# Kernel optimization log

Measured on AMD Instinct MI355X. Metric: run time of the kernel, lower is better.

Reference implementation:

```python
import jax, jax.numpy as jnp
import numpy as np

B, S, D, H = 2, 2048, 2048, 16
HD = D // H  # 128
THETA = 10000.0


def _rope_cos_sin(seq_len, head_dim):
    # matches LlamaRotaryEmbedding: inv_freq = 1/theta^(2i/d), emb = cat(freqs, freqs)
    inv_freq = 1.0 / (THETA ** (jnp.arange(0, head_dim, 2, dtype=jnp.float32) / head_dim))
    t = jnp.arange(seq_len, dtype=jnp.float32)
    freqs = jnp.einsum('s,d->sd', t, inv_freq)          # [S, HD/2]
    emb = jnp.concatenate([freqs, freqs], axis=-1)       # [S, HD]
    return jnp.cos(emb), jnp.sin(emb)


def _rotate_half(x):
    x1, x2 = jnp.split(x, 2, axis=-1)
    return jnp.concatenate([-x2, x1], axis=-1)


def setup_inputs() -> dict:
    key = jax.random.key(0)
    ks = jax.random.split(key, 5)
    scale = D ** -0.5
    x = jax.random.normal(ks[0], (B, S, D), jnp.float32)
    wq = jax.random.normal(ks[1], (D, D), jnp.float32) * scale
    wk = jax.random.normal(ks[2], (D, D), jnp.float32) * scale
    wv = jax.random.normal(ks[3], (D, D), jnp.float32) * scale
    wo = jax.random.normal(ks[4], (D, D), jnp.float32) * scale
    # additive causal mask (0 on/below diagonal, large negative above)
    causal = jnp.tril(jnp.ones((S, S), dtype=bool))
    mask = jnp.where(causal, 0.0, -1e9).astype(jnp.float32)[None, None]  # [1,1,S,S]
    return {"x": x, "wq": wq, "wk": wk, "wv": wv, "wo": wo, "mask": mask}


def reference(x, wq, wk, wv, wo, mask):
    b, s, d = x.shape
    # projections + head split: [b, H, s, HD]
    q = (x @ wq).reshape(b, s, H, HD).transpose(0, 2, 1, 3)
    k = (x @ wk).reshape(b, s, H, HD).transpose(0, 2, 1, 3)
    v = (x @ wv).reshape(b, s, H, HD).transpose(0, 2, 1, 3)
    # inline RoPE on q and k (positions 0..s-1 along the seq axis)
    cos, sin = _rope_cos_sin(s, HD)
    cos = cos[None, None]  # [1,1,s,HD]
    sin = sin[None, None]
    q = q * cos + _rotate_half(q) * sin
    k = k * cos + _rotate_half(k) * sin
    # eager attention: QK^T * scale + mask -> softmax -> @ V
    attn = jnp.einsum('bhqd,bhkd->bhqk', q, k) * (HD ** -0.5)
    attn = jax.nn.softmax(attn + mask, axis=-1)
    out = jnp.einsum('bhqk,bhkd->bhqd', attn, v)
    out = out.transpose(0, 2, 1, 3).reshape(b, s, d)
    return out @ wo
```

## Files before the change

### kernel.cpp

```cpp
#include <hip/hip_runtime.h>

#define S_LEN 2048
#define D_DIM 2048
#define NH 16
#define HD 128
#define NB 2
#define NROW (NB * S_LEN)
#define QKV_STR 6144

typedef unsigned short bf16;
typedef __attribute__((ext_vector_type(8))) short bf16x8;
typedef __attribute__((ext_vector_type(4))) float f32x4;
typedef __attribute__((ext_vector_type(16))) float f32x16;
typedef __attribute__((address_space(3))) unsigned int as3u;
typedef __attribute__((address_space(1))) unsigned int as1u;

__device__ __forceinline__ void gload16(const void* g, void* l) {
  __builtin_amdgcn_global_load_lds((const as1u*)g, (as3u*)l, 16, 0, 0);
}

__device__ __forceinline__ unsigned short f2bf(float f) {
  unsigned u = __builtin_bit_cast(unsigned, f);
  u += 0x7FFFu + ((u >> 16) & 1u);
  return (unsigned short)(u >> 16);
}
__device__ __forceinline__ float bf2f(unsigned short b) {
  return __builtin_bit_cast(float, (unsigned)b << 16);
}
__device__ __forceinline__ unsigned cvtpk(float lo, float hi) {
  unsigned r;
  asm("v_cvt_pk_bf16_f32 %0, %1, %2" : "=v"(r) : "v"(lo), "v"(hi));
  return r;
}
__device__ __forceinline__ float exp2a(float x) {
  float r;
  asm("v_exp_f32 %0, %1" : "=v"(r) : "v"(x));
  return r;
}


__global__ void rope_table_k(float2* __restrict__ tab) {
  int i = blockIdx.x * 256 + threadIdx.x;
  int s = i >> 6, d = i & 63;
  float invf = powf(10000.0f, -(float)d * (1.0f / 64.0f));
  float ang = (float)s * invf;
  tab[i] = make_float2(cosf(ang), sinf(ang));
}

__global__ void convert_x_k(const float* __restrict__ src, bf16* __restrict__ dst) {
  int i = (blockIdx.x * 256 + threadIdx.x) * 4;
  float4 v = *(const float4*)(src + i);
  ushort4 w;
  w.x = f2bf(v.x); w.y = f2bf(v.y); w.z = f2bf(v.z); w.w = f2bf(v.w);
  *(ushort4*)(dst + i) = w;
}

__global__ void transpose_w_k(const float* __restrict__ W, bf16* __restrict__ Wt) {
  __shared__ float t[64][65];
  int c0 = blockIdx.x * 64, r0 = blockIdx.y * 64;
  int tx = threadIdx.x & 63, ty = threadIdx.x >> 6;
#pragma unroll
  for (int i = 0; i < 16; ++i)
    t[ty + i * 4][tx] = W[(size_t)(r0 + ty + i * 4) * D_DIM + c0 + tx];
  __syncthreads();
#pragma unroll
  for (int i = 0; i < 16; ++i)
    Wt[(size_t)(c0 + ty + i * 4) * D_DIM + r0 + tx] = f2bf(t[tx][ty + i * 4]);
}

__global__ void transpose_v_k(const bf16* __restrict__ Vsrc, bf16* __restrict__ Vt) {
  __shared__ bf16 t[64][65];
  int bh = blockIdx.z;
  int b = bh >> 4, h = bh & 15;
  int s0 = blockIdx.x * 64, d0 = blockIdx.y * 64;
  int tx = threadIdx.x & 63, ty = threadIdx.x >> 6;
  const bf16* src = Vsrc + (size_t)(b * S_LEN + s0) * QKV_STR + h * HD + d0;
#pragma unroll
  for (int i = 0; i < 16; ++i)
    t[ty + i * 4][tx] = src[(size_t)(ty + i * 4) * QKV_STR + tx];
  __syncthreads();
  bf16* dst = Vt + ((size_t)bh * HD + d0) * S_LEN + s0;
#pragma unroll
  for (int i = 0; i < 16; ++i)
    dst[(size_t)(ty + i * 4) * S_LEN + tx] = t[tx][ty + i * 4];
}

__global__ void rope_apply_k(bf16* __restrict__ qkv, const float2* __restrict__ tab) {
  int i = blockIdx.x * 256 + threadIdx.x;
  int d = i & 63;
  int t = i >> 6;
  int h = t & 15;
  int row = t >> 4;
  int s = row & (S_LEN - 1);
  const float qscale = 0.12751743f;
  float2 cs = tab[s * 64 + d];
  size_t base = (size_t)row * QKV_STR + h * HD + d;
  float x1 = bf2f(qkv[base]), x2 = bf2f(qkv[base + 64]);
  qkv[base]      = f2bf((x1 * cs.x - x2 * cs.y) * qscale);
  qkv[base + 64] = f2bf((x2 * cs.x + x1 * cs.y) * qscale);
  size_t kb2 = base + 2048;
  float y1 = bf2f(qkv[kb2]), y2 = bf2f(qkv[kb2 + 64]);
  qkv[kb2]      = f2bf(y1 * cs.x - y2 * cs.y);
  qkv[kb2 + 64] = f2bf(y2 * cs.x + y1 * cs.y);
}


__device__ __forceinline__ void storec(bf16* p, float v) { *p = f2bf(v); }
__device__ __forceinline__ void storec(float* p, float v) { *p = v; }

template <typename OutT>
__global__ __launch_bounds__(256) void gemm_bt_k(
    const bf16* __restrict__ A, const bf16* __restrict__ Bt,
    OutT* __restrict__ C, int M, int N, int K) {
  __shared__ bf16 As[128 * 64];
  __shared__ bf16 Bs[128 * 64];
  const int tid = threadIdx.x;
  const int lane = tid & 63;
  const int wid = tid >> 6;
  const int bm = blockIdx.y * 128;
  const int bn = blockIdx.x * 128;
  const int wr = (wid >> 1) * 64;
  const int wc = (wid & 1) * 64;
  const int lr = lane & 15;
  const int kg = lane >> 4;

  f32x4 acc[4][4] = {};

  const int srow = lane >> 3;
  const int scol = ((lane & 7) ^ srow) * 8;
  const bf16* Ap = A + (size_t)(bm + wid * 32 + srow) * K + scol;
  const bf16* Bp = Bt + (size_t)(bn + wid * 32 + srow) * K + scol;
  bf16* Asd = &As[wid * 32 * 64];
  bf16* Bsd = &Bs[wid * 32 * 64];

  const int rx = (lr & 7) << 4;

  for (int k0 = 0; k0 < K; k0 += 64) {
    __syncthreads();
#pragma unroll
    for (int p = 0; p < 4; ++p) {
      gload16(Ap + (size_t)(p * 8) * K + k0, Asd + p * 8 * 64);
      gload16(Bp + (size_t)(p * 8) * K + k0, Bsd + p * 8 * 64);
    }
    __syncthreads();
    bf16x8 a[4][2], b[4][2];
#pragma unroll
    for (int m = 0; m < 4; ++m) {
      const char* rowp = (const char*)&As[(wr + m * 16 + lr) * 64];
#pragma unroll
      for (int kk = 0; kk < 2; ++kk)
        a[m][kk] = *(const bf16x8*)(rowp + ((kk * 64 + kg * 16) ^ rx));
    }
#pragma unroll
    for (int n = 0; n < 4; ++n) {
      const char* rowp = (const char*)&Bs[(wc + n * 16 + lr) * 64];
#pragma unroll
      for (int kk = 0; kk < 2; ++kk)
        b[n][kk] = *(const bf16x8*)(rowp + ((kk * 64 + kg * 16) ^ rx));
    }
#pragma unroll
    for (int kk = 0; kk < 2; ++kk)
#pragma unroll
      for (int m = 0; m < 4; ++m)
#pragma unroll
        for (int n = 0; n < 4; ++n)
          acc[m][n] = __builtin_amdgcn_mfma_f32_16x16x32_bf16(a[m][kk], b[n][kk], acc[m][n], 0, 0, 0);
  }

#pragma unroll
  for (int m = 0; m < 4; ++m) {
    int row0 = bm + wr + m * 16 + kg * 4;
#pragma unroll
    for (int n = 0; n < 4; ++n) {
      int col = bn + wc + n * 16 + lr;
#pragma unroll
      for (int r = 0; r < 4; ++r)
        storec(&C[(size_t)(row0 + r) * N + col], acc[m][n][r]);
    }
  }
}

#define FBODY(T, CUR0, CUR1, NXT0, NXT1)                                         \
  {                                                                              \
    const int kv0_ = (T) * 64;                                                   \
    stageV(kv0_ + 64, ((T) + 1) & 1);                                            \
    stageK(kv0_ + 192, kb_st);                                                   \
    kb_st = (kb_st == 2) ? 0 : kb_st + 1;                                        \
    if (kv0_ + 64 <= qw0 + 31) {                                                 \
      NXT0 = 0.0f; NXT1 = 0.0f;                                                  \
      const bf16* krow0_ = &sh[kb_rd * 8192] + (size_t)l31 * 128;                \
      const bf16* krow1_ = krow0_ + 32 * 128;                                    \
      _Pragma("unroll")                                                          \
      for (int ks = 0; ks < 8; ++ks) {                                           \
        int cb_ = ((ks * 32) ^ kxor) >> 1;                                       \
        bf16x8 kf0_ = *(const bf16x8*)(krow0_ + cb_);                            \
        bf16x8 kf1_ = *(const bf16x8*)(krow1_ + cb_);                            \
        NXT0 = __builtin_amdgcn_mfma_f32_32x32x16_bf16(kf0_, qf[ks], NXT0, 0, 0, 0); \
        NXT1 = __builtin_amdgcn_mfma_f32_32x32x16_bf16(kf1_, qf[ks], NXT1, 0, 0, 0); \
      }                                                                          \
    }                                                                            \
    kb_rd = (kb_rd == 2) ? 0 : kb_rd + 1;                                        \
    if (kv0_ <= qw0 + 31) {                                                      \
      if (kv0_ + 63 > qw0) {                                                     \
        _Pragma("unroll")                                                        \
        for (int r = 0; r < 16; ++r) {                                           \
          int kvg_ = kv0_ + (r & 3) + 8 * (r >> 2) + 4 * h;                      \
          if (kvg_ > q) CUR0[r] = -3.0e38f;                                      \
          if (kvg_ + 32 > q) CUR1[r] = -3.0e38f;                                 \
        }                                                                        \
      }                                                                          \
      float tm_[8];                                                              \
      _Pragma("unroll")                                                          \
      for (int r = 0; r < 8; ++r)                                                \
        tm_[r] = fmaxf(fmaxf(CUR0[r], CUR0[r + 8]), fmaxf(CUR1[r], CUR1[r + 8])); \
      _Pragma("unroll")                                                          \
      for (int r = 0; r < 4; ++r) tm_[r] = fmaxf(tm_[r], tm_[r + 4]);            \
      float mt_ = fmaxf(fmaxf(tm_[0], tm_[1]), fmaxf(tm_[2], tm_[3]));           \
      mt_ = fmaxf(mt_, __shfl_xor(mt_, 32));                                     \
      if (__any(mt_ > m_run + 8.0f)) {                                           \
        float mnew_ = fmaxf(m_run, mt_);                                         \
        float alpha_ = exp2a(m_run - mnew_);                                     \
        l_run *= alpha_;                                                         \
        _Pragma("unroll")                                                        \
        for (int n = 0; n < 4; ++n)                                              \
          _Pragma("unroll")                                                      \
          for (int r = 0; r < 16; ++r) ot[n][r] *= alpha_;                       \
        m_run = mnew_;                                                           \
      }                                                                          \
      float rs_[16];                                                             \
      _Pragma("unroll")                                                          \
      for (int r = 0; r < 16; ++r) {                                             \
        CUR0[r] = exp2a(CUR0[r] - m_run);                                        \
        CUR1[r] = exp2a(CUR1[r] - m_run);                                        \
        rs_[r] = CUR0[r] + CUR1[r];                                              \
      }                                                                          \
      _Pragma("unroll")                                                          \
      for (int r = 0; r < 8; ++r) rs_[r] += rs_[r + 8];                          \
      _Pragma("unroll")                                                          \
      for (int r = 0; r < 4; ++r) rs_[r] += rs_[r + 4];                          \
      float rsum_ = (rs_[0] + rs_[1]) + (rs_[2] + rs_[3]);                       \
      rsum_ += __shfl_xor(rsum_, 32);                                            \
      l_run += rsum_;                                                            \
      unsigned wd0_[8], wd1_[8];                                                 \
      _Pragma("unroll")                                                          \
      for (int j = 0; j < 8; ++j) {                                              \
        wd0_[j] = cvtpk(CUR0[2 * j], CUR0[2 * j + 1]);                           \
        wd1_[j] = cvtpk(CUR1[2 * j], CUR1[2 * j + 1]);                           \
      }                                                                          \
      const bf16* Vbuf_ = &sh[24576 + ((T) & 1) * 8192];                         \
      _Pragma("unroll")                                                          \
      for (int t4 = 0; t4 < 4; ++t4) {                                           \
        const unsigned* wdp_ = (t4 >> 1) ? wd1_ : wd0_;                          \
        int a0_ = 4 * (t4 & 1) + 2 * h;                                          \
        int sidx_ = 4 * (t4 & 1) + 2 * (1 - h);                                  \
        unsigned s0_ = (unsigned)__shfl_xor((int)wdp_[sidx_], 32);               \
        unsigned s1_ = (unsigned)__shfl_xor((int)wdp_[sidx_ + 1], 32);           \
        unsigned pb4_[4];                                                        \
        pb4_[0] = h ? s0_ : wdp_[a0_];                                           \
        pb4_[1] = h ? s1_ : wdp_[a0_ + 1];                                       \
        pb4_[2] = h ? wdp_[a0_] : s0_;                                           \
        pb4_[3] = h ? wdp_[a0_ + 1] : s1_;                                       \
        bf16x8 pb_ = __builtin_bit_cast(bf16x8, *(uint4*)pb4_);                  \
        int cb_ = ((t4 * 32) ^ vxor) >> 1;                                       \
        _Pragma("unroll")                                                        \
        for (int n = 0; n < 4; ++n) {                                            \
          bf16x8 va_ = *(const bf16x8*)(Vbuf_ + (size_t)(32 * n + l31) * 64 + cb_); \
          ot[n] = __builtin_amdgcn_mfma_f32_32x32x16_bf16(va_, pb_, ot[n], 0, 0, 0); \
        }                                                                        \
      }                                                                          \
    }                                                                            \
    asm volatile("s_waitcnt vmcnt(4)" ::: "memory");                             \
    __builtin_amdgcn_sched_barrier(0);                                           \
    __builtin_amdgcn_s_barrier();                                                \
  }

__global__ __launch_bounds__(256, 2) void flash_attn_k(
    const bf16* __restrict__ Q, const bf16* __restrict__ Kb,
    const bf16* __restrict__ Vt, bf16* __restrict__ O) {
  __shared__ bf16 sh[40960];
  const int tid = threadIdx.x;
  const int lane = tid & 63;
  const int w = tid >> 6;
  const int h = lane >> 5;
  const int l31 = lane & 31;
  const int bh = blockIdx.y;
  const int b = bh >> 4;
  const int hh = bh & 15;
  const int xr = (bh & 16) ? blockIdx.x : (gridDim.x - 1 - blockIdx.x);
  const int qb = xr * 128;
  const int qw0 = qb + 32 * w;
  const int q = qw0 + l31;

  const bf16* qp = Q + (size_t)(b * S_LEN + q) * QKV_STR + hh * HD + h * 8;
  bf16x8 qf[8];
#pragma unroll
  for (int ks = 0; ks < 8; ++ks) qf[ks] = *(const bf16x8*)(qp + ks * 16);

  f32x16 ot[4] = {};
  float m_run = -3.0e38f, l_run = 0.f;

  const bf16* Kg = Kb + (size_t)(b * S_LEN) * QKV_STR + hh * HD;
  const bf16* Vg = Vt + (size_t)bh * HD * S_LEN;

  const int kst_row = 16 * w + (lane >> 4);
  const int vst_row = 32 * w + (lane >> 3);
  const int vst_col = (((lane & 7) ^ (lane >> 3)) << 3);
  const int kxor = (16 * h) ^ ((l31 & 15) << 4);
  const int vxor = (16 * h) ^ ((l31 & 7) << 4);

  auto stageK = [&](int kv0, int buf) {
#pragma unroll
    for (int jj = 0; jj < 4; ++jj) {
      int kr = (kv0 + kst_row + jj * 4) & (S_LEN - 1);
      gload16(Kg + (size_t)kr * QKV_STR + (((lane & 15) ^ (jj * 4 + (lane >> 4))) << 3),
              &sh[buf * 8192 + (16 * w + jj * 4) * 128]);
    }
  };
  auto stageV = [&](int kv0, int buf) {
    int c = (kv0 & (S_LEN - 1)) + vst_col;
#pragma unroll
    for (int jj = 0; jj < 4; ++jj) {
      int vr = vst_row + jj * 8;
      gload16(Vg + (size_t)vr * S_LEN + c, &sh[24576 + buf * 8192 + (32 * w + jj * 8) * 64]);
    }
  };

  stageK(0, 0);
  stageV(0, 0);
  stageK(64, 1);
  stageK(128, 2);
  asm volatile("s_waitcnt vmcnt(12)" ::: "memory");
  __builtin_amdgcn_sched_barrier(0);
  __builtin_amdgcn_s_barrier();

  f32x16 stA0 = 0.0f, stA1 = 0.0f, stB0, stB1;
  {
    const bf16* krow0 = &sh[0] + (size_t)l31 * 128;
    const bf16* krow1 = krow0 + 32 * 128;
#pragma unroll
    for (int ks = 0; ks < 8; ++ks) {
      int cb = ((ks * 32) ^ kxor) >> 1;
      bf16x8 kf0 = *(const bf16x8*)(krow0 + cb);
      bf16x8 kf1 = *(const bf16x8*)(krow1 + cb);
      stA0 = __builtin_amdgcn_mfma_f32_32x32x16_bf16(kf0, qf[ks], stA0, 0, 0, 0);
      stA1 = __builtin_amdgcn_mfma_f32_32x32x16_bf16(kf1, qf[ks], stA1, 0, 0, 0);
    }
  }
  asm volatile("s_waitcnt vmcnt(4)" ::: "memory");
  __builtin_amdgcn_sched_barrier(0);
  __builtin_amdgcn_s_barrier();

  int kb_st = 0;
  int kb_rd = 1;
  const int nt = qb / 64 + 2;
  int t = 0;
  for (; t + 1 < nt; t += 2) {
    FBODY(t, stA0, stA1, stB0, stB1);
    FBODY(t + 1, stB0, stB1, stA0, stA1);
  }
  if (t < nt) FBODY(t, stA0, stA1, stB0, stB1);

  asm volatile("s_waitcnt vmcnt(0)" ::: "memory");
  __builtin_amdgcn_s_barrier();

  float inv = 1.0f / l_run;
  bf16* ow = &sh[w * 4096];
#pragma unroll
  for (int n = 0; n < 4; ++n)
#pragma unroll
    for (int rq = 0; rq < 4; ++rq) {
      int dbase = 32 * n + 8 * rq + 4 * h;
      unsigned u0 = cvtpk(ot[n][4 * rq + 0] * inv, ot[n][4 * rq + 1] * inv);
      unsigned u1 = cvtpk(ot[n][4 * rq + 2] * inv, ot[n][4 * rq + 3] * inv);
      uint2 uu = make_uint2(u0, u1);
      *(uint2*)(ow + l31 * 128 + (dbase ^ ((l31 & 15) << 3))) = uu;
    }
  __syncthreads();
#pragma unroll
  for (int p = 0; p < 8; ++p) {
    int qr = p * 4 + (lane >> 4);
    int ce = ((((lane & 15) << 4) ^ ((qr & 15) << 4)) >> 1);
    bf16x8 vrow = *(const bf16x8*)(ow + qr * 128 + ce);
    *(bf16x8*)(O + (size_t)(b * S_LEN + qw0 + qr) * D_DIM + hh * HD + (lane & 15) * 8) = vrow;
  }
}


extern "C" void kernel_launch(void* const* d_in, const int* in_sizes, int n_in,
                              void* d_out, int out_size, void* d_ws, size_t ws_size,
                              hipStream_t stream) {
  (void)in_sizes; (void)n_in; (void)out_size; (void)ws_size;
  const float* x  = (const float*)d_in[0];
  const float* wq = (const float*)d_in[1];
  const float* wk = (const float*)d_in[2];
  const float* wv = (const float*)d_in[3];
  const float* wo = (const float*)d_in[4];
  float* out = (float*)d_out;

  char* ws = (char*)d_ws;
  const size_t MB = 1u << 20;
  bf16* xb    = (bf16*)(ws + 0 * MB);
  bf16* Ob    = xb;
  bf16* wTall = (bf16*)(ws + 16 * MB);
  bf16* wTo   = (bf16*)(ws + 40 * MB);
  bf16* QKV   = (bf16*)(ws + 48 * MB);
  bf16* Vtb   = (bf16*)(ws + 96 * MB);
  float2* tab = (float2*)(ws + 112 * MB);

  rope_table_k<<<512, 256, 0, stream>>>(tab);
  convert_x_k<<<8192, 256, 0, stream>>>(x, xb);
  dim3 tg(32, 32);
  transpose_w_k<<<tg, 256, 0, stream>>>(wq, wTall);
  transpose_w_k<<<tg, 256, 0, stream>>>(wk, wTall + (size_t)2048 * D_DIM);
  transpose_w_k<<<tg, 256, 0, stream>>>(wv, wTall + (size_t)4096 * D_DIM);
  transpose_w_k<<<tg, 256, 0, stream>>>(wo, wTo);

  gemm_bt_k<bf16><<<dim3(QKV_STR / 128, NROW / 128), 256, 0, stream>>>(
      xb, wTall, QKV, NROW, QKV_STR, D_DIM);

  rope_apply_k<<<16384, 256, 0, stream>>>(QKV, tab);
  transpose_v_k<<<dim3(32, 2, 32), 256, 0, stream>>>(QKV + 4096, Vtb);

  flash_attn_k<<<dim3(S_LEN / 128, NB * NH), 256, 0, stream>>>(
      QKV, QKV + 2048, Vtb, Ob);

  gemm_bt_k<float><<<dim3(D_DIM / 128, NROW / 128), 256, 0, stream>>>(
      Ob, wTo, out, NROW, D_DIM, D_DIM);
}
```

Measured before the change: 312.1 us.

## Fuse RoPE and V transpose into QKV GEMM epilogue; batch weight transposes

Adds a dedicated QKV GEMM whose epilogue applies RoPE (plus the softmax scale on Q) and writes V straight out in transposed layout. This removes the separate rope_apply and transpose_v kernels and their extra round trips through global memory. Each warp's columns are remapped so that d and d+64 land in the same thread, which lets the rotation run in registers. The four weight-transpose launches are merged into one 3D grid launch. The V epilogue writes 4-element packed stores strided by S_LEN, and the RoPE epilogue reads the table per element, so stores may be less coalesced.

```diff
diff --git a/kernel.cpp b/kernel.cpp
--- a/kernel.cpp
+++ b/kernel.cpp
@@ -55,8 +55,13 @@
   *(ushort4*)(dst + i) = w;
 }
 
-__global__ void transpose_w_k(const float* __restrict__ W, bf16* __restrict__ Wt) {
+__global__ void transpose_w_k(const float* __restrict__ w0, const float* __restrict__ w1,
+                              const float* __restrict__ w2, const float* __restrict__ w3,
+                              bf16* __restrict__ wTall, bf16* __restrict__ wTo) {
   __shared__ float t[64][65];
+  int z = blockIdx.z;
+  const float* W = (z == 0) ? w0 : (z == 1) ? w1 : (z == 2) ? w2 : w3;
+  bf16* Wt = (z == 3) ? wTo : wTall + (size_t)z * 2048 * D_DIM;
   int c0 = blockIdx.x * 64, r0 = blockIdx.y * 64;
   int tx = threadIdx.x & 63, ty = threadIdx.x >> 6;
 #pragma unroll
@@ -66,42 +71,6 @@
 #pragma unroll
   for (int i = 0; i < 16; ++i)
     Wt[(size_t)(c0 + ty + i * 4) * D_DIM + r0 + tx] = f2bf(t[tx][ty + i * 4]);
-}
-
-__global__ void transpose_v_k(const bf16* __restrict__ Vsrc, bf16* __restrict__ Vt) {
-  __shared__ bf16 t[64][65];
-  int bh = blockIdx.z;
-  int b = bh >> 4, h = bh & 15;
-  int s0 = blockIdx.x * 64, d0 = blockIdx.y * 64;
-  int tx = threadIdx.x & 63, ty = threadIdx.x >> 6;
-  const bf16* src = Vsrc + (size_t)(b * S_LEN + s0) * QKV_STR + h * HD + d0;
-#pragma unroll
-  for (int i = 0; i < 16; ++i)
-    t[ty + i * 4][tx] = src[(size_t)(ty + i * 4) * QKV_STR + tx];
-  __syncthreads();
-  bf16* dst = Vt + ((size_t)bh * HD + d0) * S_LEN + s0;
-#pragma unroll
-  for (int i = 0; i < 16; ++i)
-    dst[(size_t)(ty + i * 4) * S_LEN + tx] = t[tx][ty + i * 4];
-}
-
-__global__ void rope_apply_k(bf16* __restrict__ qkv, const float2* __restrict__ tab) {
-  int i = blockIdx.x * 256 + threadIdx.x;
-  int d = i & 63;
-  int t = i >> 6;
-  int h = t & 15;
-  int row = t >> 4;
-  int s = row & (S_LEN - 1);
-  const float qscale = 0.12751743f;
-  float2 cs = tab[s * 64 + d];
-  size_t base = (size_t)row * QKV_STR + h * HD + d;
-  float x1 = bf2f(qkv[base]), x2 = bf2f(qkv[base + 64]);
-  qkv[base]      = f2bf((x1 * cs.x - x2 * cs.y) * qscale);
-  qkv[base + 64] = f2bf((x2 * cs.x + x1 * cs.y) * qscale);
-  size_t kb2 = base + 2048;
-  float y1 = bf2f(qkv[kb2]), y2 = bf2f(qkv[kb2 + 64]);
-  qkv[kb2]      = f2bf(y1 * cs.x - y2 * cs.y);
-  qkv[kb2 + 64] = f2bf(y2 * cs.x + y1 * cs.y);
 }
 
 
@@ -176,6 +145,105 @@
 #pragma unroll
       for (int r = 0; r < 4; ++r)
         storec(&C[(size_t)(row0 + r) * N + col], acc[m][n][r]);
+    }
+  }
+}
+
+__global__ __launch_bounds__(256) void gemm_qkv_k(
+    const bf16* __restrict__ A, const bf16* __restrict__ Bt,
+    bf16* __restrict__ QKV, bf16* __restrict__ Vt,
+    const float2* __restrict__ tab) {
+  const int K = 2048;
+  __shared__ bf16 As[128 * 64];
+  __shared__ bf16 Bs[128 * 64];
+  const int tid = threadIdx.x;
+  const int lane = tid & 63;
+  const int wid = tid >> 6;
+  const int bm = blockIdx.y * 128;
+  const int bn = blockIdx.x * 128;
+  const int wr = (wid >> 1) * 64;
+  const int wc2 = (wid & 1) * 32;
+  const int lr = lane & 15;
+  const int kg = lane >> 4;
+
+  f32x4 acc[4][4] = {};
+
+  const int srow = lane >> 3;
+  const int scol = ((lane & 7) ^ srow) * 8;
+  const bf16* Ap = A + (size_t)(bm + wid * 32 + srow) * K + scol;
+  const bf16* Bp = Bt + (size_t)(bn + wid * 32 + srow) * K + scol;
+  bf16* Asd = &As[wid * 32 * 64];
+  bf16* Bsd = &Bs[wid * 32 * 64];
+
+  const int rx = (lr & 7) << 4;
+
+  for (int k0 = 0; k0 < K; k0 += 64) {
+    __syncthreads();
+#pragma unroll
+    for (int p = 0; p < 4; ++p) {
+      gload16(Ap + (size_t)(p * 8) * K + k0, Asd + p * 8 * 64);
+      gload16(Bp + (size_t)(p * 8) * K + k0, Bsd + p * 8 * 64);
+    }
+    __syncthreads();
+    bf16x8 a[4][2], b[4][2];
+#pragma unroll
+    for (int m = 0; m < 4; ++m) {
+      const char* rowp = (const char*)&As[(wr + m * 16 + lr) * 64];
+#pragma unroll
+      for (int kk = 0; kk < 2; ++kk)
+        a[m][kk] = *(const bf16x8*)(rowp + ((kk * 64 + kg * 16) ^ rx));
+    }
+#pragma unroll
+    for (int n = 0; n < 4; ++n) {
+      int bcol = wc2 + (n & 1) * 16 + (n >> 1) * 64;
+      const char* rowp = (const char*)&Bs[(bcol + lr) * 64];
+#pragma unroll
+      for (int kk = 0; kk < 2; ++kk)
+        b[n][kk] = *(const bf16x8*)(rowp + ((kk * 64 + kg * 16) ^ rx));
+    }
+#pragma unroll
+    for (int kk = 0; kk < 2; ++kk)
+#pragma unroll
+      for (int m = 0; m < 4; ++m)
+#pragma unroll
+        for (int n = 0; n < 4; ++n)
+          acc[m][n] = __builtin_amdgcn_mfma_f32_16x16x32_bf16(a[m][kk], b[n][kk], acc[m][n], 0, 0, 0);
+  }
+
+  if (bn < 4096) {
+    const float sc = (bn < 2048) ? 0.12751743f : 1.0f;
+#pragma unroll
+    for (int m = 0; m < 4; ++m) {
+      int row0 = bm + wr + m * 16 + kg * 4;
+#pragma unroll
+      for (int j = 0; j < 2; ++j) {
+        int d = wc2 + j * 16 + lr;
+#pragma unroll
+        for (int r = 0; r < 4; ++r) {
+          int s_pos = (row0 + r) & (S_LEN - 1);
+          float2 cs = tab[s_pos * 64 + d];
+          float x1 = acc[m][j][r], x2 = acc[m][j + 2][r];
+          bf16* rowp = QKV + (size_t)(row0 + r) * QKV_STR + bn + d;
+          rowp[0]  = f2bf((x1 * cs.x - x2 * cs.y) * sc);
+          rowp[64] = f2bf((x2 * cs.x + x1 * cs.y) * sc);
+        }
+      }
+    }
+  } else {
+    int b = bm >> 11;
+    int h = (bn - 4096) >> 7;
+    bf16* vt = Vt + (size_t)(b * 16 + h) * HD * S_LEN;
+#pragma unroll
+    for (int m = 0; m < 4; ++m) {
+      int s = (bm + wr + m * 16 + kg * 4) & (S_LEN - 1);
+#pragma unroll
+      for (int n = 0; n < 4; ++n) {
+        int d = wc2 + (n & 1) * 16 + (n >> 1) * 64 + lr;
+        ushort4 pk;
+        pk.x = f2bf(acc[m][n][0]); pk.y = f2bf(acc[m][n][1]);
+        pk.z = f2bf(acc[m][n][2]); pk.w = f2bf(acc[m][n][3]);
+        *(ushort4*)(vt + (size_t)d * S_LEN + s) = pk;
+      }
     }
   }
 }
@@ -409,17 +477,10 @@
 
   rope_table_k<<<512, 256, 0, stream>>>(tab);
   convert_x_k<<<8192, 256, 0, stream>>>(x, xb);
-  dim3 tg(32, 32);
-  transpose_w_k<<<tg, 256, 0, stream>>>(wq, wTall);
-  transpose_w_k<<<tg, 256, 0, stream>>>(wk, wTall + (size_t)2048 * D_DIM);
-  transpose_w_k<<<tg, 256, 0, stream>>>(wv, wTall + (size_t)4096 * D_DIM);
-  transpose_w_k<<<tg, 256, 0, stream>>>(wo, wTo);
-
-  gemm_bt_k<bf16><<<dim3(QKV_STR / 128, NROW / 128), 256, 0, stream>>>(
-      xb, wTall, QKV, NROW, QKV_STR, D_DIM);
-
-  rope_apply_k<<<16384, 256, 0, stream>>>(QKV, tab);
-  transpose_v_k<<<dim3(32, 2, 32), 256, 0, stream>>>(QKV + 4096, Vtb);
+  transpose_w_k<<<dim3(32, 32, 4), 256, 0, stream>>>(wq, wk, wv, wo, wTall, wTo);
+
+  gemm_qkv_k<<<dim3(QKV_STR / 128, NROW / 128), 256, 0, stream>>>(
+      xb, wTall, QKV, Vtb, tab);
 
   flash_attn_k<<<dim3(S_LEN / 128, NB * NH), 256, 0, stream>>>(
       QKV, QKV + 2048, Vtb, Ob);
```

Result: faster. 286.8 us (-8.1%).
